# Kernel tuning notes

Measured on AMD Instinct MI355X. Metric: run time of the kernel, lower is better.

The kernel has to match this reference:

```python
import jax, jax.numpy as jnp
import numpy as np

N_NODES = 7823
N_DRUG = 708
N_TARGET = 1512
N_DISEASE = N_NODES - N_DRUG - N_TARGET  # 5603
FEAT = 1024
HID = 512
OUT = 256
LN_EPS = 1e-5


def _adapter_params(key, in_dim, out_dim):
    k1, k2 = jax.random.split(key)
    s1 = (2.0 / (in_dim + out_dim)) ** 0.5
    return dict(
        W=jax.random.normal(k1, (out_dim, in_dim), jnp.float32) * s1,
        b=jnp.zeros((out_dim,), jnp.float32),
        g=jnp.ones((out_dim,), jnp.float32),
        beta=jnp.zeros((out_dim,), jnp.float32),
        Wr=jax.random.normal(k2, (out_dim, in_dim), jnp.float32) * s1,
        br=jnp.zeros((out_dim,), jnp.float32),
    )


def setup_inputs() -> dict:
    key = jax.random.key(0)
    ks = jax.random.split(key, 12)
    inp = {
        'drug_feats': jax.random.normal(ks[0], (N_DRUG, FEAT), jnp.float32),
        'target_feats': jax.random.normal(ks[1], (N_TARGET, FEAT), jnp.float32),
        'disease_feats': jax.random.normal(ks[2], (N_DISEASE, FEAT), jnp.float32),
        'drug_adjs': jax.random.uniform(ks[3], (2, N_NODES, N_NODES), jnp.float32),
        'target_adjs': jax.random.uniform(ks[4], (2, N_NODES, N_NODES), jnp.float32),
    }
    # adapters
    for name, k in [('dA', ks[5]), ('tA', ks[6]), ('sA', ks[7])]:
        p = _adapter_params(k, FEAT, HID)
        for pn, pv in p.items():
            inp[name + '_' + pn] = pv
    # GCN weights: gc1 [HID,OUT], gc2 [OUT,OUT], uniform(-1/sqrt(out),1/sqrt(out))
    stdv = 1.0 / (OUT ** 0.5)
    inp['dG_W1'] = jax.random.uniform(ks[8], (HID, OUT), jnp.float32, -stdv, stdv)
    inp['dG_W2'] = jax.random.uniform(ks[9], (OUT, OUT), jnp.float32, -stdv, stdv)
    inp['tG_W1'] = jax.random.uniform(ks[10], (HID, OUT), jnp.float32, -stdv, stdv)
    inp['tG_W2'] = jax.random.uniform(ks[11], (OUT, OUT), jnp.float32, -stdv, stdv)
    inp['dG_a'] = jnp.full((1,), 0.25, jnp.float32)  # PReLU init
    inp['tG_a'] = jnp.full((1,), 0.25, jnp.float32)
    return inp


def _layernorm(x, g, b):
    m = x.mean(-1, keepdims=True)
    v = x.var(-1, keepdims=True)
    return (x - m) / jnp.sqrt(v + LN_EPS) * g + b


def _adapter(x, W, b, g, beta, Wr, br):
    out = jax.nn.relu(_layernorm(x @ W.T + b, g, beta))
    return out + x @ Wr.T + br


def _prelu(x, a):
    return jnp.where(x >= 0, x, a * x)


def _gcn(x, adj, W1, W2, a):
    h = _prelu(adj @ (x @ W1), a)
    Z = adj @ (h @ W2)
    # nn.LayerNorm(Z.size()) normalizes over the WHOLE tensor, no affine
    return (Z - Z.mean()) / jnp.sqrt(Z.var() + LN_EPS)


def reference(drug_feats, target_feats, disease_feats, drug_adjs, target_adjs,
              dA_W, dA_b, dA_g, dA_beta, dA_Wr, dA_br,
              tA_W, tA_b, tA_g, tA_beta, tA_Wr, tA_br,
              sA_W, sA_b, sA_g, sA_beta, sA_Wr, sA_br,
              dG_W1, dG_W2, dG_a, tG_W1, tG_W2, tG_a):
    h_drug = jax.nn.elu(_adapter(drug_feats, dA_W, dA_b, dA_g, dA_beta, dA_Wr, dA_br))
    h_target = jax.nn.elu(_adapter(target_feats, tA_W, tA_b, tA_g, tA_beta, tA_Wr, tA_br))
    h_disease = jax.nn.elu(_adapter(disease_feats, sA_W, sA_b, sA_g, sA_beta, sA_Wr, sA_br))
    x_all = jnp.concatenate([h_drug, h_target, h_disease], axis=0)  # [7823, HID]
    adj_d = drug_adjs.mean(0)
    adj_t = target_adjs.mean(0)
    z_drug = _gcn(x_all, adj_d, dG_W1, dG_W2, dG_a)[:N_DRUG]
    z_target = _gcn(x_all, adj_t, tG_W1, tG_W2, tG_a)[N_DRUG:N_DRUG + N_TARGET]
    z_drug = z_drug / (jnp.linalg.norm(z_drug, axis=1, keepdims=True) + 1e-8)
    z_target = z_target / (jnp.linalg.norm(z_target, axis=1, keepdims=True) + 1e-8)
    return (z_drug, z_target)
```

## Files before the change

### kernel.cpp

```cpp
#include <hip/hip_runtime.h>
#include <hip/hip_bf16.h>
#include <stdint.h>

typedef __attribute__((ext_vector_type(8))) short short8;
typedef __attribute__((ext_vector_type(4))) float f32x4;

#define N_DRUG 708
#define N_TGT  1512
#define N_NODES 7823
#define N_D_T  2220
#define KPAD   8192
#define MROWP  7936
#define NTOT   2002688
#define NSPLIT 4
#define PLANE  61199329LL
#define NCHUNK 7649917LL
#define NPADE  2886687LL
#define ADJSTR ((long long)MROWP*KPAD)
#define BTSTR  ((long long)256*KPAD)
#define PSTR   ((long long)NSPLIT*NTOT)

__device__ __forceinline__ unsigned short f2bf(float f) {
  union { float f; unsigned int i; } v; v.f = f;
  unsigned int r = v.i + 0x7FFF + ((v.i >> 16) & 1);
  return (unsigned short)(r >> 16);
}

__device__ __forceinline__ int4 pack8(const float v[8]) {
  union { int4 i4; unsigned short u[8]; } r;
  #pragma unroll
  for (int j = 0; j < 8; j++) r.u[j] = f2bf(v[j]);
  return r.i4;
}


__global__ __launch_bounds__(256) void cast_wc(
    const float* __restrict__ w0, const float* __restrict__ wr0,
    const float* __restrict__ w1, const float* __restrict__ wr1,
    const float* __restrict__ w2, const float* __restrict__ wr2,
    unsigned short* __restrict__ Wc)
{
  long long i4 = ((long long)blockIdx.x*256 + threadIdx.x)*4;
  int g  = (int)(i4 >> 20);
  int rr = (int)((i4 >> 10) & 1023);
  int c  = (int)(i4 & 1023);
  const float* src = (g==0) ? (rr<512?w0:wr0) : (g==1) ? (rr<512?w1:wr1) : (rr<512?w2:wr2);
  float4 f = *(const float4*)(src + (long long)(rr & 511)*1024 + c);
  ushort4 v; v.x=f2bf(f.x); v.y=f2bf(f.y); v.z=f2bf(f.z); v.w=f2bf(f.w);
  *(ushort4*)&Wc[i4] = v;
}

__global__ __launch_bounds__(256) void transpose_cast(
    const float* __restrict__ src, unsigned short* __restrict__ dst, int R, int C)
{
  int i = blockIdx.x*256 + threadIdx.x;
  if (i >= R*C) return;
  int r = i / C, c = i - r*C;
  dst[c*R + r] = f2bf(src[i]);
}

__global__ __launch_bounds__(256) void mean_cast2(
    const float* __restrict__ A0, const float* __restrict__ A1,
    unsigned short* __restrict__ D)
{
  const float* adj2 = blockIdx.y ? A1 : A0;
  unsigned short* dst = D + (long long)blockIdx.y * ADJSTR;
  long long stride = (long long)gridDim.x * 256;
  long long t0 = (long long)blockIdx.x*256 + threadIdx.x;
  const float* p1 = adj2 + PLANE;

  for (long long c = t0; c < NCHUNK; c += stride) {
    long long f = c*8;
    int n = (f + 8 <= PLANE) ? 8 : (int)(PLANE - f);
    float v[8];
    if (n == 8) {
      float4 a0 = *(const float4*)(adj2 + f);
      float4 a1 = *(const float4*)(adj2 + f + 4);
      float4 b0 = *(const float4*)(p1 + f);
      float4 b1 = *(const float4*)(p1 + f + 4);
      v[0]=0.5f*(a0.x+b0.x); v[1]=0.5f*(a0.y+b0.y);
      v[2]=0.5f*(a0.z+b0.z); v[3]=0.5f*(a0.w+b0.w);
      v[4]=0.5f*(a1.x+b1.x); v[5]=0.5f*(a1.y+b1.y);
      v[6]=0.5f*(a1.z+b1.z); v[7]=0.5f*(a1.w+b1.w);
    } else {
      #pragma unroll
      for (int j=0;j<8;j++) v[j] = (j<n) ? 0.5f*(adj2[f+j]+p1[f+j]) : 0.f;
    }
    int row = (int)(f / 7823LL);
    int col = (int)(f - (long long)row*7823LL);
    if (n == 8 && col + 8 <= 7823) {
      unsigned short* d = dst + (long long)row*KPAD + col;
      #pragma unroll
      for (int j=0;j<8;j++) d[j] = f2bf(v[j]);
    } else {
      #pragma unroll
      for (int j=0;j<8;j++) {
        if (j < n) {
          long long ff = f + j;
          int r2 = (int)(ff / 7823LL);
          int c2 = (int)(ff - (long long)r2*7823LL);
          dst[(long long)r2*KPAD + c2] = f2bf(v[j]);
        }
      }
    }
  }
  for (long long i = t0; i < NPADE; i += stride) {
    int r = (int)(i / 369LL);
    int c2 = 7823 + (int)(i - (long long)r*369LL);
    dst[(long long)r*KPAD + c2] = 0;
  }
}

__global__ __launch_bounds__(512, 2) void spmmK(
    const unsigned short* __restrict__ Abase,
    const unsigned short* __restrict__ Bbase,
    float* __restrict__ parts)
{
  __shared__ __align__(16) unsigned short Bs[128*256];

  int nwg = gridDim.x;
  int bid = (blockIdx.x & 7)*(nwg >> 3) + (blockIdx.x >> 3);
  int b  = bid / 248;
  int r  = bid % 248;
  int ks = r / 62;
  int q  = r % 62;
  int mt = q >> 1, nt = q & 1;

  const unsigned short* A  = Abase + b*ADJSTR;
  const unsigned short* BT = Bbase + b*BTSTR;
  int m0 = mt*256, n0 = nt*128;
  int kt0 = ks*32;

  int tid = threadIdx.x, lane = tid & 63, w = tid >> 6;
  long long rA0 = (long long)(m0 + w*32 + (lane&15))*KPAD + (lane>>4)*8;

  f32x4 acc[2][8] = {};

  int srow[8], sslot[8];
  #pragma unroll
  for (int i=0;i<8;i++){ int c = i*512 + tid; srow[i] = c>>5; sslot[i] = c&31; }

  int4 breg[8];
  auto loadB = [&](int sub){
    long long kb = (long long)kt0*64 + sub*256;
    #pragma unroll
    for (int i=0;i<8;i++)
      breg[i] = *(const int4*)(BT + (long long)(n0+srow[i])*KPAD + kb + sslot[i]*8);
  };
  auto storeB = [&](){
    #pragma unroll
    for (int i=0;i<8;i++)
      *(int4*)(Bs + srow[i]*256 + (sslot[i]^(srow[i]&7))*8) = breg[i];
  };
  auto loadA = [&](int g, int4* a){
    const unsigned short* p = A + rA0 + (long long)g*64;
    a[0] = *(const int4*)(p);
    a[1] = *(const int4*)(p + 16*KPAD);
    a[2] = *(const int4*)(p + 32);
    a[3] = *(const int4*)(p + 16*KPAD + 32);
  };
  auto compute = [&](int lt, const int4* a){
    #pragma unroll
    for (int kk=0; kk<2; ++kk) {
      short8 bv[8];
      #pragma unroll
      for (int nf=0; nf<8; ++nf) {
        int row = nf*16 + (lane&15);
        int sl  = (lt*8 + kk*4 + (lane>>4)) ^ (lane&7);
        bv[nf] = *(const short8*)&Bs[row*256 + sl*8];
      }
      #pragma unroll
      for (int mf=0; mf<2; ++mf) {
        short8 av = *(const short8*)&a[kk*2+mf];
        #pragma unroll
        for (int nf=0; nf<8; ++nf)
          acc[mf][nf] = __builtin_amdgcn_mfma_f32_16x16x32_bf16(av, bv[nf], acc[mf][nf], 0, 0, 0);
      }
    }
  };

  int4 a0[4], a1[4];
  loadB(0);
  loadA(kt0, a0);
  int gmax = kt0 + 31;

  for (int sub = 0; sub < 8; ++sub) {
    __syncthreads();
    storeB();
    __syncthreads();
    if (sub < 7) loadB(sub+1);
    int g = kt0 + sub*4;
    loadA(min(g+1,gmax), a1); compute(0, a0);
    loadA(min(g+2,gmax), a0); compute(1, a1);
    loadA(min(g+3,gmax), a1); compute(2, a0);
    loadA(min(g+4,gmax), a0); compute(3, a1);
  }

  float* P = parts + b*PSTR + (long long)ks*NTOT;
  #pragma unroll
  for (int mf=0; mf<2; ++mf) {
    int mb = m0 + w*32 + mf*16 + ((lane>>4)<<2);
    #pragma unroll
    for (int i=0;i<4;i++){
      int m = mb + i;
      if (m < N_NODES) {
        #pragma unroll
        for (int nf=0; nf<8; ++nf) {
          int n = n0 + nf*16 + (lane&15);
          P[(long long)m*256 + n] = acc[mf][nf][i];
        }
      }
    }
  }
}

#define BN 256
#define BK 64

__global__ __launch_bounds__(512, 4) void gemmS(
    const unsigned short* __restrict__ Abase, long long a_bstr, int lda,
    const unsigned short* __restrict__ Bbase, long long b_bstr, int ldb,
    int m_cnt, int tiles_m, int ktiles,
    unsigned short* __restrict__ CTb, long long ct_bstr, int ldct)
{
  __shared__ __align__(16) unsigned short As[64*BK];
  __shared__ __align__(16) unsigned short Bs[BN*BK];

  int bid = blockIdx.x;
  int b   = bid / tiles_m;
  int tm  = bid % tiles_m;

  const unsigned short* A  = Abase + b*a_bstr;
  const unsigned short* BT = Bbase + b*b_bstr;

  int m0 = tm*64;
  int tid = threadIdx.x;
  int lane = tid & 63, w = tid >> 6;
  int wm = (w >> 2)*32, wn = (w & 3)*64;

  f32x4 acc[2][4] = {};

  int arow, aslot, brow[4], bslot[4];
  { int c = tid; arow = c>>3; aslot = c&7; }
  #pragma unroll
  for (int i=0;i<4;i++){ int c = i*512 + tid; brow[i] = c>>3; bslot[i] = c&7; }

  int4 ra, rb[4];
  auto loadAB = [&](int kt){
    int gr = m0 + arow; if (gr > m_cnt-1) gr = m_cnt-1;
    ra = *(const int4*)(A + (long long)gr*lda + kt*BK + aslot*8);
    #pragma unroll
    for (int i=0;i<4;i++)
      rb[i] = *(const int4*)(BT + (long long)brow[i]*ldb + kt*BK + bslot[i]*8);
  };
  auto storeAB = [&](){
    *(int4*)(As + arow*BK + (aslot^(arow&7))*8) = ra;
    #pragma unroll
    for (int i=0;i<4;i++)
      *(int4*)(Bs + brow[i]*BK + (bslot[i]^(brow[i]&7))*8) = rb[i];
  };

  loadAB(0);
  for (int kt = 0; kt < ktiles; ++kt) {
    __syncthreads();
    storeAB();
    __syncthreads();
    if (kt+1 < ktiles) loadAB(kt+1);
    #pragma unroll
    for (int kk=0; kk<2; ++kk) {
      short8 av[2], bv[4];
      #pragma unroll
      for (int x=0;x<2;x++){
        int row = wm + x*16 + (lane&15);
        int slot = kk*4 + (lane>>4);
        av[x] = *(const short8*)&As[row*BK + (slot^(row&7))*8];
      }
      #pragma unroll
      for (int x=0;x<4;x++){
        int row = wn + x*16 + (lane&15);
        int slot = kk*4 + (lane>>4);
        bv[x] = *(const short8*)&Bs[row*BK + (slot^(row&7))*8];
      }
      #pragma unroll
      for (int mf=0; mf<2; ++mf)
        #pragma unroll
        for (int nf=0; nf<4; ++nf)
          acc[mf][nf] = __builtin_amdgcn_mfma_f32_16x16x32_bf16(av[mf], bv[nf], acc[mf][nf], 0, 0, 0);
    }
  }

  unsigned short* CT = CTb + b*ct_bstr;
  #pragma unroll
  for (int nf=0; nf<4; ++nf) {
    int n = wn + nf*16 + (lane&15);
    #pragma unroll
    for (int mf=0; mf<2; ++mf) {
      int mb = m0 + wm + mf*16 + ((lane>>4)<<2);
      ushort4 v;
      v.x = (mb+0 < m_cnt) ? f2bf(acc[mf][nf][0]) : (unsigned short)0;
      v.y = (mb+1 < m_cnt) ? f2bf(acc[mf][nf][1]) : (unsigned short)0;
      v.z = (mb+2 < m_cnt) ? f2bf(acc[mf][nf][2]) : (unsigned short)0;
      v.w = (mb+3 < m_cnt) ? f2bf(acc[mf][nf][3]) : (unsigned short)0;
      *(ushort4*)&CT[(long long)n*ldct + mb] = v;
    }
  }
}

__global__ __launch_bounds__(512, 4) void adapt_gemm(
    const float* __restrict__ f0, const float* __restrict__ f1, const float* __restrict__ f2,
    const unsigned short* __restrict__ Wc, float* __restrict__ C1)
{
  __shared__ __align__(16) unsigned short As[64*BK];
  __shared__ __align__(16) unsigned short Bs[BN*BK];

  int bid = blockIdx.x;
  int tn = bid & 3, tq = bid >> 2;
  int g, lt, m_cnt, gstart;
  if (tq < 12)      { g=0; lt=tq;    m_cnt=N_DRUG;           gstart=0; }
  else if (tq < 36) { g=1; lt=tq-12; m_cnt=N_TGT;            gstart=N_DRUG; }
  else              { g=2; lt=tq-36; m_cnt=N_NODES-N_D_T;    gstart=N_D_T; }
  const float* A = (g==0) ? f0 : (g==1) ? f1 : f2;
  const unsigned short* BT = Wc + (long long)g*1024*1024;

  int m0 = lt*64, n0 = tn*BN;
  int tid = threadIdx.x;
  int lane = tid & 63, w = tid >> 6;
  int wm = (w >> 2)*32, wn = (w & 3)*64;

  f32x4 acc[2][4] = {};

  int arow, aslot, brow[4], bslot[4];
  { int c = tid; arow = c>>3; aslot = c&7; }
  #pragma unroll
  for (int i=0;i<4;i++){ int c = i*512 + tid; brow[i] = c>>3; bslot[i] = c&7; }

  int4 ra, rb[4];
  auto loadAB = [&](int kt){
    int gr = m0 + arow; if (gr > m_cnt-1) gr = m_cnt-1;
    const float* p = A + (long long)gr*1024 + kt*BK + aslot*8;
    float4 q0 = *(const float4*)p;
    float4 q1 = *(const float4*)(p+4);
    float v[8] = {q0.x,q0.y,q0.z,q0.w,q1.x,q1.y,q1.z,q1.w};
    ra = pack8(v);
    #pragma unroll
    for (int i=0;i<4;i++)
      rb[i] = *(const int4*)(BT + (long long)(n0 + brow[i])*1024 + kt*BK + bslot[i]*8);
  };
  auto storeAB = [&](){
    *(int4*)(As + arow*BK + (aslot^(arow&7))*8) = ra;
    #pragma unroll
    for (int i=0;i<4;i++)
      *(int4*)(Bs + brow[i]*BK + (bslot[i]^(brow[i]&7))*8) = rb[i];
  };

  loadAB(0);
  for (int kt = 0; kt < 16; ++kt) {
    __syncthreads();
    storeAB();
    __syncthreads();
    if (kt+1 < 16) loadAB(kt+1);
    #pragma unroll
    for (int kk=0; kk<2; ++kk) {
      short8 av[2], bv[4];
      #pragma unroll
      for (int x=0;x<2;x++){
        int row = wm + x*16 + (lane&15);
        int slot = kk*4 + (lane>>4);
        av[x] = *(const short8*)&As[row*BK + (slot^(row&7))*8];
      }
      #pragma unroll
      for (int x=0;x<4;x++){
        int row = wn + x*16 + (lane&15);
        int slot = kk*4 + (lane>>4);
        bv[x] = *(const short8*)&Bs[row*BK + (slot^(row&7))*8];
      }
      #pragma unroll
      for (int mf=0; mf<2; ++mf)
        #pragma unroll
        for (int nf=0; nf<4; ++nf)
          acc[mf][nf] = __builtin_amdgcn_mfma_f32_16x16x32_bf16(av[mf], bv[nf], acc[mf][nf], 0, 0, 0);
    }
  }

  #pragma unroll
  for (int mf=0; mf<2; ++mf) {
    int mb = m0 + wm + mf*16 + ((lane>>4)<<2);
    #pragma unroll
    for (int i=0;i<4;i++){
      int m = mb + i;
      if (m < m_cnt) {
        #pragma unroll
        for (int nf=0; nf<4; ++nf) {
          int n = n0 + wn + nf*16 + (lane&15);
          C1[(long long)(gstart+m)*1024 + n] = acc[mf][nf][i];
        }
      }
    }
  }
}


__global__ __launch_bounds__(256) void adapter_fuse(
    const float* __restrict__ C1,
    const float* __restrict__ b0, const float* __restrict__ g0, const float* __restrict__ be0, const float* __restrict__ br0,
    const float* __restrict__ b1, const float* __restrict__ g1, const float* __restrict__ be1, const float* __restrict__ br1,
    const float* __restrict__ b2, const float* __restrict__ g2, const float* __restrict__ be2, const float* __restrict__ br2,
    unsigned short* __restrict__ xall)
{
  int r = blockIdx.x;
  const float *b, *g, *be, *br;
  if (r < N_DRUG)     { b=b0; g=g0; be=be0; br=br0; }
  else if (r < N_D_T) { b=b1; g=g1; be=be1; br=br1; }
  else                { b=b2; g=g2; be=be2; br=br2; }
  int t = threadIdx.x;
  const float* row = C1 + (long long)r*1024;
  float ya = row[t]       + b[t];
  float yb = row[t + 256] + b[t + 256];
  float s = ya + yb, q = ya*ya + yb*yb;
  #pragma unroll
  for (int o=32;o;o>>=1){ s += __shfl_down(s,o); q += __shfl_down(q,o); }
  __shared__ float ss[4], qq[4];
  if ((t & 63) == 0) { ss[t>>6]=s; qq[t>>6]=q; }
  __syncthreads();
  float S = ss[0]+ss[1]+ss[2]+ss[3];
  float Q = qq[0]+qq[1]+qq[2]+qq[3];
  float mean = S * (1.f/512.f);
  float var  = Q * (1.f/512.f) - mean*mean;
  float inv  = rsqrtf(var + 1e-5f);
  float za = fmaxf((ya-mean)*inv*g[t]     + be[t],     0.f);
  float zb = fmaxf((yb-mean)*inv*g[t+256] + be[t+256], 0.f);
  float ha = za + row[512 + t] + br[t];
  float hb = zb + row[768 + t] + br[t + 256];
  ha = (ha > 0.f) ? ha : (expf(ha) - 1.f);
  hb = (hb > 0.f) ? hb : (expf(hb) - 1.f);
  xall[(long long)r*512 + t]       = f2bf(ha);
  xall[(long long)r*512 + t + 256] = f2bf(hb);
}

__global__ __launch_bounds__(256) void reduce_prelu2(
    const float* __restrict__ parts, const float* __restrict__ a0, const float* __restrict__ a1,
    unsigned short* __restrict__ h)
{
  int b = blockIdx.y;
  long long i = (long long)blockIdx.x*256 + threadIdx.x;
  const float* P = parts + b*PSTR;
  float s = 0.f;
  #pragma unroll
  for (int p=0;p<NSPLIT;p++) s += P[(long long)p*NTOT + i];
  float a = (b ? a1 : a0)[0];
  h[b*(long long)NTOT + i] = f2bf(s >= 0.f ? s : a*s);
}

__global__ __launch_bounds__(256) void reduce_stats2(
    const float* __restrict__ parts, float* __restrict__ Z, float* __restrict__ sp)
{
  int b = blockIdx.y;
  long long i = (long long)blockIdx.x*256 + threadIdx.x;
  const float* P = parts + b*PSTR;
  float s = 0.f;
  #pragma unroll
  for (int p=0;p<NSPLIT;p++) s += P[(long long)p*NTOT + i];
  Z[b*(long long)NTOT + i] = s;
  float a = s, q = s*s;
  #pragma unroll
  for (int o=32;o;o>>=1){ a += __shfl_down(a,o); q += __shfl_down(q,o); }
  __shared__ float ss[4], qq[4];
  int t = threadIdx.x;
  if ((t&63)==0){ ss[t>>6]=a; qq[t>>6]=q; }
  __syncthreads();
  if (t==0) {
    sp[(long long)b*2*N_NODES + 2*blockIdx.x]   = ss[0]+ss[1]+ss[2]+ss[3];
    sp[(long long)b*2*N_NODES + 2*blockIdx.x+1] = qq[0]+qq[1]+qq[2]+qq[3];
  }
}

__global__ __launch_bounds__(256) void stats_final2(
    const float* __restrict__ sp, float* __restrict__ stats)
{
  int b = blockIdx.x;
  const float* S = sp + (long long)b*2*N_NODES;
  int t = threadIdx.x;
  float s = 0.f, q = 0.f;
  for (int i=t; i<N_NODES; i+=256){ s += S[2*i]; q += S[2*i+1]; }
  #pragma unroll
  for (int o=32;o;o>>=1){ s += __shfl_down(s,o); q += __shfl_down(q,o); }
  __shared__ float ss[4], qq[4];
  if ((t&63)==0){ ss[t>>6]=s; qq[t>>6]=q; }
  __syncthreads();
  if (t==0){ stats[b*16]=ss[0]+ss[1]+ss[2]+ss[3]; stats[b*16+1]=qq[0]+qq[1]+qq[2]+qq[3]; }
}

__global__ __launch_bounds__(256) void finalize(
    const float* __restrict__ Z, const float* __restrict__ stats,
    float* __restrict__ out, int row_lo, long long out_off)
{
  int r = row_lo + blockIdx.x;
  int t = threadIdx.x;
  float mean = stats[0] * (1.f/(float)NTOT);
  float var  = stats[1] * (1.f/(float)NTOT) - mean*mean;
  float inv  = rsqrtf(var + 1e-5f);
  float z = (Z[(long long)r*256 + t] - mean) * inv;
  float q = z*z;
  #pragma unroll
  for (int o=32;o;o>>=1) q += __shfl_down(q,o);
  __shared__ float qq[4];
  if ((t&63)==0) qq[t>>6]=q;
  __syncthreads();
  float norm = sqrtf(qq[0]+qq[1]+qq[2]+qq[3]);
  out[out_off + (long long)blockIdx.x*256 + t] = z / (norm + 1e-8f);
}


extern "C" void kernel_launch(void* const* d_in, const int* in_sizes, int n_in,
                              void* d_out, int out_size, void* d_ws, size_t ws_size,
                              hipStream_t stream)
{
  const float* drug_feats    = (const float*)d_in[0];
  const float* target_feats  = (const float*)d_in[1];
  const float* disease_feats = (const float*)d_in[2];
  const float* drug_adjs     = (const float*)d_in[3];
  const float* target_adjs   = (const float*)d_in[4];
  const float* dA_W  = (const float*)d_in[5];
  const float* dA_b  = (const float*)d_in[6];
  const float* dA_g  = (const float*)d_in[7];
  const float* dA_be = (const float*)d_in[8];
  const float* dA_Wr = (const float*)d_in[9];
  const float* dA_br = (const float*)d_in[10];
  const float* tA_W  = (const float*)d_in[11];
  const float* tA_b  = (const float*)d_in[12];
  const float* tA_g  = (const float*)d_in[13];
  const float* tA_be = (const float*)d_in[14];
  const float* tA_Wr = (const float*)d_in[15];
  const float* tA_br = (const float*)d_in[16];
  const float* sA_W  = (const float*)d_in[17];
  const float* sA_b  = (const float*)d_in[18];
  const float* sA_g  = (const float*)d_in[19];
  const float* sA_be = (const float*)d_in[20];
  const float* sA_Wr = (const float*)d_in[21];
  const float* sA_br = (const float*)d_in[22];
  const float* dG_W1 = (const float*)d_in[23];
  const float* dG_W2 = (const float*)d_in[24];
  const float* tG_W1 = (const float*)d_in[25];
  const float* tG_W2 = (const float*)d_in[26];
  const float* dG_a  = (const float*)d_in[27];
  const float* tG_a  = (const float*)d_in[28];

  char* ws = (char*)d_ws;
  size_t off = 0;
  auto alloc = [&](size_t bytes)->void* {
    void* p = ws + off;
    off += (bytes + 255) & ~(size_t)255;
    return p;
  };

  unsigned short* Wc   = (unsigned short*)alloc((size_t)3*1024*1024*2);
  unsigned short* W1T  = (unsigned short*)alloc((size_t)2*256*512*2);
  unsigned short* W2T  = (unsigned short*)alloc((size_t)2*256*256*2);
  unsigned short* xall = (unsigned short*)alloc((size_t)N_NODES*512*2);
  unsigned short* adjb = (unsigned short*)alloc((size_t)2*ADJSTR*2);
  unsigned short* xw1T = (unsigned short*)alloc((size_t)2*BTSTR*2);
  unsigned short* hbuf = (unsigned short*)alloc((size_t)2*NTOT*2);
  unsigned short* hw2T = (unsigned short*)alloc((size_t)2*BTSTR*2);
  float* parts = (float*)alloc((size_t)2*PSTR*4);
  float* Zf    = (float*)alloc((size_t)2*NTOT*4);
  float* spart = (float*)alloc((size_t)2*N_NODES*2*4);
  float* stats = (float*)alloc((size_t)32*4);
  float* C1    = parts;
  float* outp  = (float*)d_out;

  cast_wc<<<3072, 256, 0, stream>>>(dA_W, dA_Wr, tA_W, tA_Wr, sA_W, sA_Wr, Wc);
  transpose_cast<<<512, 256, 0, stream>>>(dG_W1, W1T,            512, 256);
  transpose_cast<<<512, 256, 0, stream>>>(tG_W1, W1T + 256*512,  512, 256);
  transpose_cast<<<256, 256, 0, stream>>>(dG_W2, W2T,            256, 256);
  transpose_cast<<<256, 256, 0, stream>>>(tG_W2, W2T + 256*256,  256, 256);

  adapt_gemm<<<496, 512, 0, stream>>>(drug_feats, target_feats, disease_feats, Wc, C1);
  adapter_fuse<<<N_NODES, 256, 0, stream>>>(C1,
      dA_b, dA_g, dA_be, dA_br,
      tA_b, tA_g, tA_be, tA_br,
      sA_b, sA_g, sA_be, sA_br, xall);

  gemmS<<<2*128, 512, 0, stream>>>(
      xall, 0, 512, W1T, 256*512, 512,
      N_NODES, 128, 8, xw1T, BTSTR, KPAD);

  mean_cast2<<<dim3(2048,2), 256, 0, stream>>>(drug_adjs, target_adjs, adjb);

  spmmK<<<496, 512, 0, stream>>>(adjb, xw1T, parts);

  reduce_prelu2<<<dim3(N_NODES,2), 256, 0, stream>>>(parts, dG_a, tG_a, hbuf);

  gemmS<<<2*128, 512, 0, stream>>>(
      hbuf, (long long)NTOT, 256, W2T, 256*256, 256,
      N_NODES, 128, 4, hw2T, BTSTR, KPAD);

  spmmK<<<496, 512, 0, stream>>>(adjb, hw2T, parts);

  reduce_stats2<<<dim3(N_NODES,2), 256, 0, stream>>>(parts, Zf, spart);
  stats_final2<<<2, 256, 0, stream>>>(spart, stats);

  finalize<<<N_DRUG, 256, 0, stream>>>(Zf, stats, outp, 0, 0LL);
  finalize<<<N_TGT, 256, 0, stream>>>(Zf + NTOT, stats + 16, outp, N_DRUG, (long long)N_DRUG*256);
}
```

Measured before the change: 907.7 us.

## Fuse adjacency mean-cast into first SpMM and retile to full-N blocks

Removes the separate mean_cast2 pass. The first SpMM now reads both fp32 adjacency planes directly, averages them and converts to bf16 in registers for the MFMA. It also writes the bf16 result to the side buffer so the second SpMM can reuse it. The SpMM tiling changes from 256x128 tiles to 128x256 (full N per block), so each A tile is read once and no longer once per N half. This trades one extra write/read round trip of the adjacency for heavier fp32 loads inside the GEMM and a longer dependency chain in its main loop, and zero padding columns are no longer written explicitly beyond the tile reads.

Result: slower. 1.188 ms (+30.9%).

```diff
diff --git a/kernel.cpp b/kernel.cpp
--- a/kernel.cpp
+++ b/kernel.cpp
@@ -14,8 +14,6 @@
 #define NTOT   2002688
 #define NSPLIT 4
 #define PLANE  61199329LL
-#define NCHUNK 7649917LL
-#define NPADE  2886687LL
 #define ADJSTR ((long long)MROWP*KPAD)
 #define BTSTR  ((long long)256*KPAD)
 #define PSTR   ((long long)NSPLIT*NTOT)
@@ -59,115 +57,132 @@
   dst[c*R + r] = f2bf(src[i]);
 }
 
-__global__ __launch_bounds__(256) void mean_cast2(
-    const float* __restrict__ A0, const float* __restrict__ A1,
-    unsigned short* __restrict__ D)
-{
-  const float* adj2 = blockIdx.y ? A1 : A0;
-  unsigned short* dst = D + (long long)blockIdx.y * ADJSTR;
-  long long stride = (long long)gridDim.x * 256;
-  long long t0 = (long long)blockIdx.x*256 + threadIdx.x;
-  const float* p1 = adj2 + PLANE;
-
-  for (long long c = t0; c < NCHUNK; c += stride) {
-    long long f = c*8;
-    int n = (f + 8 <= PLANE) ? 8 : (int)(PLANE - f);
-    float v[8];
-    if (n == 8) {
-      float4 a0 = *(const float4*)(adj2 + f);
-      float4 a1 = *(const float4*)(adj2 + f + 4);
-      float4 b0 = *(const float4*)(p1 + f);
-      float4 b1 = *(const float4*)(p1 + f + 4);
-      v[0]=0.5f*(a0.x+b0.x); v[1]=0.5f*(a0.y+b0.y);
-      v[2]=0.5f*(a0.z+b0.z); v[3]=0.5f*(a0.w+b0.w);
-      v[4]=0.5f*(a1.x+b1.x); v[5]=0.5f*(a1.y+b1.y);
-      v[6]=0.5f*(a1.z+b1.z); v[7]=0.5f*(a1.w+b1.w);
-    } else {
-      #pragma unroll
-      for (int j=0;j<8;j++) v[j] = (j<n) ? 0.5f*(adj2[f+j]+p1[f+j]) : 0.f;
-    }
-    int row = (int)(f / 7823LL);
-    int col = (int)(f - (long long)row*7823LL);
-    if (n == 8 && col + 8 <= 7823) {
-      unsigned short* d = dst + (long long)row*KPAD + col;
-      #pragma unroll
-      for (int j=0;j<8;j++) d[j] = f2bf(v[j]);
-    } else {
-      #pragma unroll
-      for (int j=0;j<8;j++) {
-        if (j < n) {
-          long long ff = f + j;
-          int r2 = (int)(ff / 7823LL);
-          int c2 = (int)(ff - (long long)r2*7823LL);
-          dst[(long long)r2*KPAD + c2] = f2bf(v[j]);
-        }
-      }
-    }
-  }
-  for (long long i = t0; i < NPADE; i += stride) {
-    int r = (int)(i / 369LL);
-    int c2 = 7823 + (int)(i - (long long)r*369LL);
-    dst[(long long)r*KPAD + c2] = 0;
-  }
-}
-
+template<int AMODE>
 __global__ __launch_bounds__(512, 2) void spmmK(
     const unsigned short* __restrict__ Abase,
+    const float* __restrict__ F0, const float* __restrict__ F1,
+    unsigned short* __restrict__ sideW,
     const unsigned short* __restrict__ Bbase,
     float* __restrict__ parts)
 {
-  __shared__ __align__(16) unsigned short Bs[128*256];
-
-  int nwg = gridDim.x;
-  int bid = (blockIdx.x & 7)*(nwg >> 3) + (blockIdx.x >> 3);
+  __shared__ __align__(16) unsigned short Bs[256*128];
+
+  int bid = (blockIdx.x & 7)*62 + (blockIdx.x >> 3);
   int b  = bid / 248;
   int r  = bid % 248;
   int ks = r / 62;
-  int q  = r % 62;
-  int mt = q >> 1, nt = q & 1;
-
-  const unsigned short* A  = Abase + b*ADJSTR;
+  int mt = r % 62;
+
   const unsigned short* BT = Bbase + b*BTSTR;
-  int m0 = mt*256, n0 = nt*128;
+  int m0 = mt*128;
   int kt0 = ks*32;
 
   int tid = threadIdx.x, lane = tid & 63, w = tid >> 6;
-  long long rA0 = (long long)(m0 + w*32 + (lane&15))*KPAD + (lane>>4)*8;
+  int grow  = m0 + (w>>1)*32 + (lane&15);
+  int wn    = (w&1)*128;
+  int klane = (lane>>4)*8;
 
   f32x4 acc[2][8] = {};
 
   int srow[8], sslot[8];
   #pragma unroll
-  for (int i=0;i<8;i++){ int c = i*512 + tid; srow[i] = c>>5; sslot[i] = c&31; }
+  for (int i=0;i<8;i++){ int c = i*512 + tid; srow[i] = c>>4; sslot[i] = c&15; }
 
   int4 breg[8];
   auto loadB = [&](int sub){
-    long long kb = (long long)kt0*64 + sub*256;
+    long long kb = (long long)kt0*64 + sub*128;
     #pragma unroll
     for (int i=0;i<8;i++)
-      breg[i] = *(const int4*)(BT + (long long)(n0+srow[i])*KPAD + kb + sslot[i]*8);
+      breg[i] = *(const int4*)(BT + (long long)srow[i]*KPAD + kb + sslot[i]*8);
   };
   auto storeB = [&](){
     #pragma unroll
     for (int i=0;i<8;i++)
-      *(int4*)(Bs + srow[i]*256 + (sslot[i]^(srow[i]&7))*8) = breg[i];
-  };
-  auto loadA = [&](int g, int4* a){
+      *(int4*)(Bs + srow[i]*128 + (sslot[i]^(srow[i]&7))*8) = breg[i];
+  };
+
+  const unsigned short* A = Abase + b*ADJSTR;
+  long long rA0 = (long long)grow*KPAD + klane;
+  const float* F = (AMODE==2) ? (b ? F1 : F0) : nullptr;
+  unsigned short* SW = (AMODE==2) ? (sideW + b*ADJSTR) : nullptr;
+
+  int4 a0[4], a1[4];
+  float4 fr[16];
+  int4 av2[4];
+
+  auto loadA0 = [&](int g, int4* a){
     const unsigned short* p = A + rA0 + (long long)g*64;
     a[0] = *(const int4*)(p);
     a[1] = *(const int4*)(p + 16*KPAD);
     a[2] = *(const int4*)(p + 32);
     a[3] = *(const int4*)(p + 16*KPAD + 32);
   };
+  auto loadF = [&](int g){
+    if (g <= 121) {
+      #pragma unroll
+      for (int fi=0; fi<4; ++fi){
+        int mf = fi & 1, kk = fi >> 1;
+        int gr = grow + mf*16; if (gr > N_NODES-1) gr = N_NODES-1;
+        long long kg = (long long)g*64 + kk*32 + klane;
+        const float* p0 = F + (long long)gr*N_NODES + kg;
+        fr[fi*4+0] = *(const float4*)p0;
+        fr[fi*4+1] = *(const float4*)(p0+4);
+        fr[fi*4+2] = *(const float4*)(p0+PLANE);
+        fr[fi*4+3] = *(const float4*)(p0+PLANE+4);
+      }
+    } else if (g == 122) {
+      #pragma unroll
+      for (int fi=0; fi<4; ++fi){
+        int mf = fi & 1, kk = fi >> 1;
+        int gr = grow + mf*16; if (gr > N_NODES-1) gr = N_NODES-1;
+        long long kg = (long long)g*64 + kk*32 + klane;
+        const float* p0 = F + (long long)gr*N_NODES;
+        float ta[8], tb[8];
+        #pragma unroll
+        for (int j=0;j<8;j++){
+          long long k = kg + j;
+          bool ok = (k < N_NODES);
+          ta[j] = ok ? p0[k] : 0.f;
+          tb[j] = ok ? p0[PLANE + k] : 0.f;
+        }
+        fr[fi*4+0] = make_float4(ta[0],ta[1],ta[2],ta[3]);
+        fr[fi*4+1] = make_float4(ta[4],ta[5],ta[6],ta[7]);
+        fr[fi*4+2] = make_float4(tb[0],tb[1],tb[2],tb[3]);
+        fr[fi*4+3] = make_float4(tb[4],tb[5],tb[6],tb[7]);
+      }
+    } else {
+      #pragma unroll
+      for (int i=0;i<16;i++) fr[i] = make_float4(0.f,0.f,0.f,0.f);
+    }
+  };
+  auto convF = [&](){
+    #pragma unroll
+    for (int fi=0; fi<4; ++fi){
+      float4 x0 = fr[fi*4+0], x1 = fr[fi*4+1];
+      float4 y0 = fr[fi*4+2], y1 = fr[fi*4+3];
+      float v[8] = {0.5f*(x0.x+y0.x), 0.5f*(x0.y+y0.y), 0.5f*(x0.z+y0.z), 0.5f*(x0.w+y0.w),
+                    0.5f*(x1.x+y1.x), 0.5f*(x1.y+y1.y), 0.5f*(x1.z+y1.z), 0.5f*(x1.w+y1.w)};
+      av2[fi] = pack8(v);
+    }
+  };
+  auto sideWrite = [&](int g){
+    #pragma unroll
+    for (int fi=0; fi<4; ++fi){
+      int mf = fi & 1, kk = fi >> 1;
+      int gr = grow + mf*16;
+      if (gr < N_NODES)
+        *(int4*)(SW + (long long)gr*KPAD + (long long)g*64 + kk*32 + klane) = av2[fi];
+    }
+  };
   auto compute = [&](int lt, const int4* a){
     #pragma unroll
     for (int kk=0; kk<2; ++kk) {
       short8 bv[8];
       #pragma unroll
       for (int nf=0; nf<8; ++nf) {
-        int row = nf*16 + (lane&15);
-        int sl  = (lt*8 + kk*4 + (lane>>4)) ^ (lane&7);
-        bv[nf] = *(const short8*)&Bs[row*256 + sl*8];
+        int row = wn + nf*16 + (lane&15);
+        int sl  = (lt*8 + kk*4 + (lane>>4)) ^ (row&7);
+        bv[nf] = *(const short8*)&Bs[row*128 + sl*8];
       }
       #pragma unroll
       for (int mf=0; mf<2; ++mf) {
@@ -179,34 +194,42 @@
     }
   };
 
-  int4 a0[4], a1[4];
   loadB(0);
-  loadA(kt0, a0);
-  int gmax = kt0 + 31;
-
-  for (int sub = 0; sub < 8; ++sub) {
+  if (AMODE == 0) { loadA0(kt0, a0); loadA0(kt0+1, a1); }
+  else            { loadF(kt0); }
+
+  for (int sub = 0; sub < 16; ++sub) {
     __syncthreads();
     storeB();
     __syncthreads();
-    if (sub < 7) loadB(sub+1);
-    int g = kt0 + sub*4;
-    loadA(min(g+1,gmax), a1); compute(0, a0);
-    loadA(min(g+2,gmax), a0); compute(1, a1);
-    loadA(min(g+3,gmax), a1); compute(2, a0);
-    loadA(min(g+4,gmax), a0); compute(3, a1);
+    if (sub < 15) loadB(sub+1);
+    int g = kt0 + sub*2;
+    if (AMODE == 0) {
+      compute(0, a0);
+      if (g+2 < kt0+32) loadA0(g+2, a0);
+      compute(1, a1);
+      if (g+3 < kt0+32) loadA0(g+3, a1);
+    } else {
+      convF(); sideWrite(g);
+      loadF(g+1);
+      compute(0, av2);
+      convF(); sideWrite(g+1);
+      if (g+2 < kt0+32) loadF(g+2);
+      compute(1, av2);
+    }
   }
 
   float* P = parts + b*PSTR + (long long)ks*NTOT;
   #pragma unroll
   for (int mf=0; mf<2; ++mf) {
-    int mb = m0 + w*32 + mf*16 + ((lane>>4)<<2);
+    int mb = m0 + (w>>1)*32 + mf*16 + ((lane>>4)<<2);
     #pragma unroll
     for (int i=0;i<4;i++){
       int m = mb + i;
       if (m < N_NODES) {
         #pragma unroll
         for (int nf=0; nf<8; ++nf) {
-          int n = n0 + nf*16 + (lane&15);
+          int n = wn + nf*16 + (lane&15);
           P[(long long)m*256 + n] = acc[mf][nf][i];
         }
       }
@@ -584,9 +607,7 @@
       xall, 0, 512, W1T, 256*512, 512,
       N_NODES, 128, 8, xw1T, BTSTR, KPAD);
 
-  mean_cast2<<<dim3(2048,2), 256, 0, stream>>>(drug_adjs, target_adjs, adjb);
-
-  spmmK<<<496, 512, 0, stream>>>(adjb, xw1T, parts);
+  spmmK<2><<<496, 512, 0, stream>>>(adjb, drug_adjs, target_adjs, adjb, xw1T, parts);
 
   reduce_prelu2<<<dim3(N_NODES,2), 256, 0, stream>>>(parts, dG_a, tG_a, hbuf);
 
@@ -594,7 +615,7 @@
       hbuf, (long long)NTOT, 256, W2T, 256*256, 256,
       N_NODES, 128, 4, hw2T, BTSTR, KPAD);
 
-  spmmK<<<496, 512, 0, stream>>>(adjb, hw2T, parts);
+  spmmK<0><<<496, 512, 0, stream>>>(adjb, nullptr, nullptr, nullptr, hw2T, parts);
 
   reduce_stats2<<<dim3(N_NODES,2), 256, 0, stream>>>(parts, Zf, spart);
   stats_final2<<<2, 256, 0, stream>>>(spart, stats);
```

## Double-buffer B tiles in spmmK and rewrite adjacency mean-cast per row

Applied to the files above, without the earlier changes.

The spmmK kernel now keeps two shared-memory B buffers, so the next B sub-tile is stored while the current one is consumed. It also prefetches four A fragments ahead instead of two, and replaces __syncthreads with explicit barriers and waitcnt. Separately, the adjacency mean-and-cast kernel changes from a flat grid-stride loop with per-element row/column division to one block per row, using packed 16-byte bf16 stores. Risks: the doubled LDS footprint (128KB per block) likely prevents two blocks per CU. The new cast no longer writes zeros into the padding columns, and it issues float4 loads from rows that are not 16-byte aligned.

New measurement: 841.4 us, median of 2. 7.3% less time.

```diff
diff --git a/kernel.cpp b/kernel.cpp
--- a/kernel.cpp
+++ b/kernel.cpp
@@ -14,8 +14,6 @@
 #define NTOT   2002688
 #define NSPLIT 4
 #define PLANE  61199329LL
-#define NCHUNK 7649917LL
-#define NPADE  2886687LL
 #define ADJSTR ((long long)MROWP*KPAD)
 #define BTSTR  ((long long)256*KPAD)
 #define PSTR   ((long long)NSPLIT*NTOT)
@@ -59,55 +57,28 @@
   dst[c*R + r] = f2bf(src[i]);
 }
 
-__global__ __launch_bounds__(256) void mean_cast2(
+__global__ __launch_bounds__(256) void mean_cast_row(
     const float* __restrict__ A0, const float* __restrict__ A1,
     unsigned short* __restrict__ D)
 {
-  const float* adj2 = blockIdx.y ? A1 : A0;
-  unsigned short* dst = D + (long long)blockIdx.y * ADJSTR;
-  long long stride = (long long)gridDim.x * 256;
-  long long t0 = (long long)blockIdx.x*256 + threadIdx.x;
-  const float* p1 = adj2 + PLANE;
-
-  for (long long c = t0; c < NCHUNK; c += stride) {
-    long long f = c*8;
-    int n = (f + 8 <= PLANE) ? 8 : (int)(PLANE - f);
-    float v[8];
-    if (n == 8) {
-      float4 a0 = *(const float4*)(adj2 + f);
-      float4 a1 = *(const float4*)(adj2 + f + 4);
-      float4 b0 = *(const float4*)(p1 + f);
-      float4 b1 = *(const float4*)(p1 + f + 4);
-      v[0]=0.5f*(a0.x+b0.x); v[1]=0.5f*(a0.y+b0.y);
-      v[2]=0.5f*(a0.z+b0.z); v[3]=0.5f*(a0.w+b0.w);
-      v[4]=0.5f*(a1.x+b1.x); v[5]=0.5f*(a1.y+b1.y);
-      v[6]=0.5f*(a1.z+b1.z); v[7]=0.5f*(a1.w+b1.w);
-    } else {
-      #pragma unroll
-      for (int j=0;j<8;j++) v[j] = (j<n) ? 0.5f*(adj2[f+j]+p1[f+j]) : 0.f;
-    }
-    int row = (int)(f / 7823LL);
-    int col = (int)(f - (long long)row*7823LL);
-    if (n == 8 && col + 8 <= 7823) {
-      unsigned short* d = dst + (long long)row*KPAD + col;
-      #pragma unroll
-      for (int j=0;j<8;j++) d[j] = f2bf(v[j]);
-    } else {
-      #pragma unroll
-      for (int j=0;j<8;j++) {
-        if (j < n) {
-          long long ff = f + j;
-          int r2 = (int)(ff / 7823LL);
-          int c2 = (int)(ff - (long long)r2*7823LL);
-          dst[(long long)r2*KPAD + c2] = f2bf(v[j]);
-        }
-      }
-    }
-  }
-  for (long long i = t0; i < NPADE; i += stride) {
-    int r = (int)(i / 369LL);
-    int c2 = 7823 + (int)(i - (long long)r*369LL);
-    dst[(long long)r*KPAD + c2] = 0;
+  int row = blockIdx.x;
+  const float* p0 = (blockIdx.y ? A1 : A0) + (long long)row*N_NODES;
+  const float* p1 = p0 + PLANE;
+  unsigned short* d = D + (long long)blockIdx.y*ADJSTR + (long long)row*KPAD;
+
+  for (int c = threadIdx.x*8; c < 7816; c += 2048) {
+    float4 a0 = *(const float4*)(p0+c);
+    float4 a1 = *(const float4*)(p0+c+4);
+    float4 b0 = *(const float4*)(p1+c);
+    float4 b1 = *(const float4*)(p1+c+4);
+    float v[8] = {0.5f*(a0.x+b0.x), 0.5f*(a0.y+b0.y), 0.5f*(a0.z+b0.z), 0.5f*(a0.w+b0.w),
+                  0.5f*(a1.x+b1.x), 0.5f*(a1.y+b1.y), 0.5f*(a1.z+b1.z), 0.5f*(a1.w+b1.w)};
+    *(int4*)(d + c) = pack8(v);
+  }
+  int t = threadIdx.x;
+  if (t < 7) {
+    int c = 7816 + t;
+    d[c] = f2bf(0.5f*(p0[c] + p1[c]));
   }
 }
 
@@ -116,14 +87,13 @@
     const unsigned short* __restrict__ Bbase,
     float* __restrict__ parts)
 {
-  __shared__ __align__(16) unsigned short Bs[128*256];
-
-  int nwg = gridDim.x;
-  int bid = (blockIdx.x & 7)*(nwg >> 3) + (blockIdx.x >> 3);
-  int b  = bid / 248;
-  int r  = bid % 248;
-  int ks = r / 62;
-  int q  = r % 62;
+  __shared__ __align__(16) unsigned short Bs[2][128*256];
+
+  int bid = (blockIdx.x & 7)*62 + (blockIdx.x >> 3);
+  int grp = bid / 62;
+  int q   = bid % 62;
+  int b  = grp >> 2;
+  int ks = grp & 3;
   int mt = q >> 1, nt = q & 1;
 
   const unsigned short* A  = Abase + b*ADJSTR;
@@ -132,7 +102,8 @@
   int kt0 = ks*32;
 
   int tid = threadIdx.x, lane = tid & 63, w = tid >> 6;
-  long long rA0 = (long long)(m0 + w*32 + (lane&15))*KPAD + (lane>>4)*8;
+  int grow = m0 + w*32 + (lane&15);
+  long long rA0 = (long long)grow*KPAD + (lane>>4)*8;
 
   f32x4 acc[2][8] = {};
 
@@ -147,10 +118,10 @@
     for (int i=0;i<8;i++)
       breg[i] = *(const int4*)(BT + (long long)(n0+srow[i])*KPAD + kb + sslot[i]*8);
   };
-  auto storeB = [&](){
+  auto storeB = [&](unsigned short* buf){
     #pragma unroll
     for (int i=0;i<8;i++)
-      *(int4*)(Bs + srow[i]*256 + (sslot[i]^(srow[i]&7))*8) = breg[i];
+      *(int4*)(buf + srow[i]*256 + (sslot[i]^(srow[i]&7))*8) = breg[i];
   };
   auto loadA = [&](int g, int4* a){
     const unsigned short* p = A + rA0 + (long long)g*64;
@@ -159,7 +130,7 @@
     a[2] = *(const int4*)(p + 32);
     a[3] = *(const int4*)(p + 16*KPAD + 32);
   };
-  auto compute = [&](int lt, const int4* a){
+  auto compute = [&](int lt, const int4* a, const unsigned short* buf){
     #pragma unroll
     for (int kk=0; kk<2; ++kk) {
       short8 bv[8];
@@ -167,7 +138,7 @@
       for (int nf=0; nf<8; ++nf) {
         int row = nf*16 + (lane&15);
         int sl  = (lt*8 + kk*4 + (lane>>4)) ^ (lane&7);
-        bv[nf] = *(const short8*)&Bs[row*256 + sl*8];
+        bv[nf] = *(const short8*)&buf[row*256 + sl*8];
       }
       #pragma unroll
       for (int mf=0; mf<2; ++mf) {
@@ -179,21 +150,38 @@
     }
   };
 
-  int4 a0[4], a1[4];
+  int gmax = kt0 + 31;
+  int4 a0[4], a1[4], a2[4], a3[4];
+
   loadB(0);
-  loadA(kt0, a0);
-  int gmax = kt0 + 31;
-
+  loadA(kt0+0, a0);
+  loadA(kt0+1, a1);
+  loadA(kt0+2, a2);
+  loadA(kt0+3, a3);
+  storeB(&Bs[0][0]);
+  loadB(1);
+  asm volatile("s_waitcnt lgkmcnt(0)" ::: "memory");
+  __builtin_amdgcn_s_barrier();
+  __builtin_amdgcn_sched_barrier(0);
+
+  int cur = 0;
   for (int sub = 0; sub < 8; ++sub) {
-    __syncthreads();
-    storeB();
-    __syncthreads();
-    if (sub < 7) loadB(sub+1);
+    const unsigned short* Bc = &Bs[cur][0];
     int g = kt0 + sub*4;
-    loadA(min(g+1,gmax), a1); compute(0, a0);
-    loadA(min(g+2,gmax), a0); compute(1, a1);
-    loadA(min(g+3,gmax), a1); compute(2, a0);
-    loadA(min(g+4,gmax), a0); compute(3, a1);
+    compute(0, a0, Bc); loadA(min(g+4, gmax), a0);
+    compute(1, a1, Bc); loadA(min(g+5, gmax), a1);
+    compute(2, a2, Bc); loadA(min(g+6, gmax), a2);
+    compute(3, a3, Bc); loadA(min(g+7, gmax), a3);
+    if (sub < 7) {
+      __builtin_amdgcn_s_barrier();
+      __builtin_amdgcn_sched_barrier(0);
+      storeB(&Bs[cur^1][0]);
+      loadB(min(sub+2, 7));
+      asm volatile("s_waitcnt lgkmcnt(0)" ::: "memory");
+      __builtin_amdgcn_s_barrier();
+      __builtin_amdgcn_sched_barrier(0);
+      cur ^= 1;
+    }
   }
 
   float* P = parts + b*PSTR + (long long)ks*NTOT;
@@ -584,7 +572,7 @@
       xall, 0, 512, W1T, 256*512, 512,
       N_NODES, 128, 8, xw1T, BTSTR, KPAD);
 
-  mean_cast2<<<dim3(2048,2), 256, 0, stream>>>(drug_adjs, target_adjs, adjb);
+  mean_cast_row<<<dim3(N_NODES, 2), 256, 0, stream>>>(drug_adjs, target_adjs, adjb);
 
   spmmK<<<496, 512, 0, stream>>>(adjb, xw1T, parts);
 
```
